# Kernel tuning notes

Hardware: AMD Instinct MI355X
Metric: run time of the kernel (lower is better)

The kernel has to match this reference:

```python
import jax, jax.numpy as jnp
import numpy as np

NUM_HEAD = 16
DIM_HEAD = 64
IN_DIM = NUM_HEAD * DIM_HEAD
SLEN = 1024
BSZ = 32
LN_EPS = 1e-5


def setup_inputs() -> dict:
    key = jax.random.key(0)
    ks = jax.random.split(key, 8)
    std = 1.0 / np.sqrt(DIM_HEAD)
    std_q = 0.01 / np.sqrt(DIM_HEAD)
    h = jax.random.normal(ks[0], (SLEN, BSZ, IN_DIM), dtype=jnp.float32)
    W_y = std * jax.random.normal(ks[1], (1, NUM_HEAD, DIM_HEAD, DIM_HEAD), dtype=jnp.float32)
    W_q = std_q * jax.random.normal(ks[2], (1, NUM_HEAD, DIM_HEAD, DIM_HEAD), dtype=jnp.float32)
    W_k = std * jax.random.normal(ks[3], (1, NUM_HEAD, DIM_HEAD, DIM_HEAD), dtype=jnp.float32)
    w_b = -1.0 + std * jax.random.normal(ks[4], (1, NUM_HEAD, DIM_HEAD, 4), dtype=jnp.float32)
    out_w = (1.0 / np.sqrt(IN_DIM)) * jax.random.normal(ks[5], (IN_DIM, IN_DIM), dtype=jnp.float32)  # (out, in), no bias
    ln_g = jnp.ones((IN_DIM,), dtype=jnp.float32)
    ln_b = jnp.zeros((IN_DIM,), dtype=jnp.float32)
    return {"h": h, "W_y": W_y, "W_q": W_q, "W_k": W_k, "w_b": w_b,
            "out_w": out_w, "ln_g": ln_g, "ln_b": ln_b}


def _layer_norm(x, g, b):
    mu = jnp.mean(x, axis=-1, keepdims=True)
    var = jnp.mean(jnp.square(x - mu), axis=-1, keepdims=True)
    return (x - mu) * jax.lax.rsqrt(var + LN_EPS) * g + b


def _srwm_forward(h, W_y, W_q, W_k, w_b, out_w, ln_g, ln_b):
    slen, bsz, in_dim = h.shape
    H, D = W_y.shape[1], W_y.shape[2]
    x = h.reshape(slen, bsz, H, D)  # (T,B,H,D) -- scan over leading T

    Wy0 = jnp.broadcast_to(W_y, (bsz, H, D, D))
    Wq0 = jnp.broadcast_to(W_q, (bsz, H, D, D))
    Wk0 = jnp.broadcast_to(W_k, (bsz, H, D, D))
    wb0 = jnp.broadcast_to(w_b, (bsz, H, D, 4))

    def step(carry, x_t):
        Wy, Wq, Wk, wb = carry  # (B,H,D,D) / (B,H,D,4)
        y = jnp.einsum('bhod,bhd->bho', Wy, x_t)
        q = jax.nn.softmax(jnp.einsum('bhod,bhd->bho', Wq, x_t), axis=-1)
        k = jax.nn.softmax(jnp.einsum('bhod,bhd->bho', Wk, x_t), axis=-1)
        beta = jax.nn.sigmoid(jnp.einsum('bhdk,bhd->bhk', wb, x_t))  # (B,H,4)
        # old values (keyed by k) and new target values (keyed by q)
        yk = jnp.einsum('bhod,bhd->bho', Wy, k); yq = jnp.einsum('bhod,bhd->bho', Wy, q)
        qk = jnp.einsum('bhod,bhd->bho', Wq, k); qq = jnp.einsum('bhod,bhd->bho', Wq, q)
        kk = jnp.einsum('bhod,bhd->bho', Wk, k); kq = jnp.einsum('bhod,bhd->bho', Wk, q)
        bk = jnp.einsum('bhdk,bhd->bhk', wb, k); bq = jnp.einsum('bhdk,bhd->bhk', wb, q)
        # delta-rule rank-1 self-modification, per-submatrix learned rate
        Wy = Wy + beta[..., 0, None, None] * ((yq - yk)[..., :, None] * k[..., None, :])
        Wq = Wq + beta[..., 1, None, None] * ((qq - qk)[..., :, None] * k[..., None, :])
        Wk = Wk + beta[..., 2, None, None] * ((kq - kk)[..., :, None] * k[..., None, :])
        wb = wb + beta[..., 3, None, None] * (k[..., :, None] * (bq - bk)[..., None, :])
        out_t = jax.nn.softmax(y, axis=-1)  # v0 applies softmax on y
        return (Wy, Wq, Wk, wb), out_t

    _, ys = jax.lax.scan(step, (Wy0, Wq0, Wk0, wb0), x)  # ys: (T,B,H,D)
    out = ys.reshape(slen, bsz, H * D)
    out = out @ out_w.T  # out_linear, no bias
    out = _layer_norm(h, ln_g, ln_b) + out  # use_ln + use_res
    return out


def reference(h, W_y, W_q, W_k, w_b, out_w, ln_g, ln_b):
    return _srwm_forward(h, W_y, W_q, W_k, w_b, out_w, ln_g, ln_b)
```

## Files before the change

kernel.cpp:

```cpp
#include <hip/hip_runtime.h>
#include <hip/hip_bf16.h>

#define SLEN 1024
#define BSZ 32
#define NHEAD 16
#define DHEAD 64
#define INDIM 1024

typedef __attribute__((ext_vector_type(8))) __bf16 bf16x8;
typedef __attribute__((ext_vector_type(4))) float f32x4;
typedef __attribute__((ext_vector_type(2))) float f32x2;

#if __has_builtin(__builtin_elementwise_fma)
__device__ __forceinline__ f32x2 pk_fma(f32x2 a, f32x2 b, f32x2 c) {
  return __builtin_elementwise_fma(a, b, c);
}
#else
__device__ __forceinline__ f32x2 pk_fma(f32x2 a, f32x2 b, f32x2 c) {
  f32x2 r; r.x = fmaf(a.x, b.x, c.x); r.y = fmaf(a.y, b.y, c.y); return r;
}
#endif

template <int C>
__device__ __forceinline__ float dppmov(float v) {
  return __int_as_float(__builtin_amdgcn_update_dpp(
      __float_as_int(v), __float_as_int(v), C, 0xF, 0xF, false));
}
__device__ __forceinline__ float wred_sum_u(float v) {
  v += dppmov<0x111>(v);
  v += dppmov<0x112>(v);
  v += dppmov<0x114>(v);
  v += dppmov<0x118>(v);
  v += dppmov<0x142>(v);
  v += dppmov<0x143>(v);
  return __int_as_float(__builtin_amdgcn_readlane(__float_as_int(v), 63));
}
__device__ __forceinline__ float wred_max_u(float v) {
  v = fmaxf(v, dppmov<0x111>(v));
  v = fmaxf(v, dppmov<0x112>(v));
  v = fmaxf(v, dppmov<0x114>(v));
  v = fmaxf(v, dppmov<0x118>(v));
  v = fmaxf(v, dppmov<0x142>(v));
  v = fmaxf(v, dppmov<0x143>(v));
  return __int_as_float(__builtin_amdgcn_readlane(__float_as_int(v), 63));
}

__global__ __launch_bounds__(256, 2) void srwm_scan(
    const float* __restrict__ h,
    const float* __restrict__ Wy0, const float* __restrict__ Wq0,
    const float* __restrict__ Wk0, const float* __restrict__ wb0,
    __hip_bfloat16* __restrict__ ys)
{
  const int p  = blockIdx.x;
  const int b  = p >> 4;
  const int hd = p & 15;
  const int tid = threadIdx.x;
  const int w = tid >> 6, l = tid & 63;

  __shared__ float sx[2][64];
  __shared__ float sq[2][64];
  __shared__ float sk[2][64];
  __shared__ float sbeta[2][4];

  f32x2 wrow[32];
  float xnext = 0.f;
  float cshift = 0.f;

  if (w < 3) {
    const float* base = (w == 0) ? Wy0 : (w == 1) ? Wq0 : Wk0;
    const float4* s4 = (const float4*)(base + (size_t)(hd * DHEAD + l) * DHEAD);
#pragma unroll
    for (int c = 0; c < 16; ++c) {
      const float4 v = s4[c];
      wrow[2 * c + 0] = f32x2{v.x, v.y};
      wrow[2 * c + 1] = f32x2{v.z, v.w};
    }
  } else {
    const float4 v = *(const float4*)(wb0 + (size_t)(hd * DHEAD + l) * 4);
    wrow[0] = f32x2{v.x, v.y};
    wrow[1] = f32x2{v.z, v.w};
    sx[0][l] = h[(size_t)b * INDIM + hd * DHEAD + l];
    xnext = h[(size_t)BSZ * INDIM + (size_t)b * INDIM + hd * DHEAD + l];
  }
  __syncthreads();

  const size_t xstride = (size_t)BSZ * INDIM;
  const float* xsrc = h + (size_t)b * INDIM + hd * DHEAD + l;
  __hip_bfloat16* ydst = ys + (size_t)b * INDIM + hd * DHEAD + l;

#pragma unroll 2
  for (int t = 0; t < SLEN; ++t) {
    const int cur = t & 1, nxt = cur ^ 1;
    if (w < 3) {
      const float* xb = sx[cur];
      f32x2 a0 = (f32x2)(0.f), a1 = (f32x2)(0.f);
#pragma unroll
      for (int c = 0; c < 16; ++c) {
        const float4 xc = *(const float4*)(xb + 4 * c);
        a0 = pk_fma(wrow[2 * c + 0], f32x2{xc.x, xc.y}, a0);
        a1 = pk_fma(wrow[2 * c + 1], f32x2{xc.z, xc.w}, a1);
      }
      const f32x2 as = a0 + a1;
      const float a = as.x + as.y;
      const float e = __expf(a - cshift);
      const float mnew = wred_max_u(a);
      const float s = wred_sum_u(e);
      const float sm = e * __builtin_amdgcn_rcpf(s);
      cshift = mnew;
      if (w == 0) {
        ydst[(size_t)t * xstride] = __float2bfloat16(sm);
      } else if (w == 1) {
        sq[cur][l] = sm;
      } else {
        sk[cur][l] = sm;
      }
    } else {
      sx[nxt][l] = xnext;
      const int tload = (t + 2 < SLEN) ? (t + 2) : (SLEN - 1);
      xnext = xsrc[(size_t)tload * xstride];
      const float xd = sx[cur][l];
      const float z0 = wred_sum_u(wrow[0].x * xd);
      const float z1 = wred_sum_u(wrow[0].y * xd);
      const float z2 = wred_sum_u(wrow[1].x * xd);
      const float z3 = wred_sum_u(wrow[1].y * xd);
      if (l == 0) {
        sbeta[cur][0] = __builtin_amdgcn_rcpf(1.f + __expf(-z0));
        sbeta[cur][1] = __builtin_amdgcn_rcpf(1.f + __expf(-z1));
        sbeta[cur][2] = __builtin_amdgcn_rcpf(1.f + __expf(-z2));
        sbeta[cur][3] = __builtin_amdgcn_rcpf(1.f + __expf(-z3));
      }
    }
    __syncthreads();
    if (w < 3) {
      const float* qb = sq[cur];
      const float* kb = sk[cur];
      const float beta = sbeta[cur][w];
      f32x2 kr[32];
      f32x2 d0 = (f32x2)(0.f), d1 = (f32x2)(0.f);
#pragma unroll
      for (int c = 0; c < 16; ++c) {
        const float4 q4 = *(const float4*)(qb + 4 * c);
        const float4 k4 = *(const float4*)(kb + 4 * c);
        const f32x2 klo = f32x2{k4.x, k4.y}, khi = f32x2{k4.z, k4.w};
        kr[2 * c + 0] = klo; kr[2 * c + 1] = khi;
        d0 = pk_fma(wrow[2 * c + 0], f32x2{q4.x, q4.y} - klo, d0);
        d1 = pk_fma(wrow[2 * c + 1], f32x2{q4.z, q4.w} - khi, d1);
      }
      const f32x2 dsum = d0 + d1;
      const float sc = beta * (dsum.x + dsum.y);
      const f32x2 scv = (f32x2)(sc);
#pragma unroll
      for (int c = 0; c < 32; ++c) wrow[c] = pk_fma(scv, kr[c], wrow[c]);
    } else {
      const float qd = sq[cur][l], kd = sk[cur][l];
      const float dd = qd - kd;
      const float z0 = wred_sum_u(wrow[0].x * dd);
      const float z1 = wred_sum_u(wrow[0].y * dd);
      const float z2 = wred_sum_u(wrow[1].x * dd);
      const float z3 = wred_sum_u(wrow[1].y * dd);
      const float s3 = sbeta[cur][3] * kd;
      wrow[0].x = fmaf(s3, z0, wrow[0].x);
      wrow[0].y = fmaf(s3, z1, wrow[0].y);
      wrow[1].x = fmaf(s3, z2, wrow[1].x);
      wrow[1].y = fmaf(s3, z3, wrow[1].y);
    }
  }
}

__global__ __launch_bounds__(256) void ln_stats(
    const float* __restrict__ h, float2* __restrict__ stats)
{
  const int row = blockIdx.x * 4 + (threadIdx.x >> 6);
  const int l = threadIdx.x & 63;
  const float4* hp = (const float4*)(h + (size_t)row * INDIM);
  float s = 0.f, s2 = 0.f;
#pragma unroll
  for (int c = 0; c < 4; ++c) {
    const float4 v = hp[c * 64 + l];
    s  += v.x + v.y + v.z + v.w;
    s2 += v.x * v.x + v.y * v.y + v.z * v.z + v.w * v.w;
  }
  s  = wred_sum_u(s);
  s2 = wred_sum_u(s2);
  if (l == 0) {
    const float mu  = s * (1.f / INDIM);
    const float var = s2 * (1.f / INDIM) - mu * mu;
    stats[row] = make_float2(mu, rsqrtf(var + 1e-5f));
  }
}

__global__ void cvt_bf16(const float* __restrict__ src,
                         __hip_bfloat16* __restrict__ dst, int n)
{
  const int i = blockIdx.x * blockDim.x + threadIdx.x;
  if (i < n) dst[i] = __float2bfloat16(src[i]);
}

__global__ __launch_bounds__(256) void gemm_ln(
    const __hip_bfloat16* __restrict__ A,
    const __hip_bfloat16* __restrict__ Bw,
    const float* __restrict__ h,
    const float2* __restrict__ stats,
    const float* __restrict__ g,
    const float* __restrict__ bvec,
    float* __restrict__ out)
{
  const int K = INDIM;
  __shared__ __align__(16) __hip_bfloat16 As[128 * 32];
  __shared__ __align__(16) __hip_bfloat16 Bs[128 * 32];
  const int tid = threadIdx.x, w = tid >> 6, l = tid & 63;
  const int wm = w >> 1, wn = w & 1;
  const int m0 = blockIdx.x * 128, n0 = blockIdx.y * 128;

  f32x4 acc[4][4];
#pragma unroll
  for (int i = 0; i < 4; ++i)
#pragma unroll
    for (int j = 0; j < 4; ++j) acc[i][j] = (f32x4)(0.f);

  const int mr = tid >> 2;
  const int kc = (tid & 3) * 8;

  for (int k0 = 0; k0 < K; k0 += 32) {
    const uint4 va0 = *(const uint4*)(A  + (size_t)(m0 + mr)      * K + k0 + kc);
    const uint4 va1 = *(const uint4*)(A  + (size_t)(m0 + mr + 64) * K + k0 + kc);
    const uint4 vb0 = *(const uint4*)(Bw + (size_t)(n0 + mr)      * K + k0 + kc);
    const uint4 vb1 = *(const uint4*)(Bw + (size_t)(n0 + mr + 64) * K + k0 + kc);
    *(uint4*)((char*)As + (size_t)tid * 16)         = va0;
    *(uint4*)((char*)As + (size_t)(tid + 256) * 16) = va1;
    *(uint4*)((char*)Bs + (size_t)tid * 16)         = vb0;
    *(uint4*)((char*)Bs + (size_t)(tid + 256) * 16) = vb1;
    __syncthreads();

    bf16x8 af[4], bfr[4];
    const int koff = (l >> 4) * 16;
#pragma unroll
    for (int i = 0; i < 4; ++i) {
      af[i]  = *(const bf16x8*)((const char*)As +
                 (size_t)(wm * 64 + i * 16 + (l & 15)) * 64 + koff);
      bfr[i] = *(const bf16x8*)((const char*)Bs +
                 (size_t)(wn * 64 + i * 16 + (l & 15)) * 64 + koff);
    }
#pragma unroll
    for (int i = 0; i < 4; ++i)
#pragma unroll
      for (int j = 0; j < 4; ++j)
        acc[i][j] = __builtin_amdgcn_mfma_f32_16x16x32_bf16(
            af[i], bfr[j], acc[i][j], 0, 0, 0);
    __syncthreads();
  }

  float gv[4], bv[4];
  int cols[4];
#pragma unroll
  for (int j = 0; j < 4; ++j) {
    const int col = n0 + wn * 64 + j * 16 + (l & 15);
    cols[j] = col; gv[j] = g[col]; bv[j] = bvec[col];
  }
#pragma unroll
  for (int i = 0; i < 4; ++i) {
#pragma unroll
    for (int r = 0; r < 4; ++r) {
      const int row = m0 + wm * 64 + i * 16 + (l >> 4) * 4 + r;
      const float2 st = stats[row];
      const float* hrow = h + (size_t)row * INDIM;
      float* orow = out + (size_t)row * INDIM;
#pragma unroll
      for (int j = 0; j < 4; ++j) {
        const float lnv = (hrow[cols[j]] - st.x) * st.y * gv[j] + bv[j];
        orow[cols[j]] = acc[i][j][r] + lnv;
      }
    }
  }
}

extern "C" void kernel_launch(void* const* d_in, const int* in_sizes, int n_in,
                              void* d_out, int out_size, void* d_ws, size_t ws_size,
                              hipStream_t stream)
{
  const float* h    = (const float*)d_in[0];
  const float* Wy   = (const float*)d_in[1];
  const float* Wq   = (const float*)d_in[2];
  const float* Wk   = (const float*)d_in[3];
  const float* wb   = (const float*)d_in[4];
  const float* outw = (const float*)d_in[5];
  const float* lng  = (const float*)d_in[6];
  const float* lnb  = (const float*)d_in[7];
  float* out = (float*)d_out;

  char* ws = (char*)d_ws;
  __hip_bfloat16* ys  = (__hip_bfloat16*)ws;
  __hip_bfloat16* wbf = (__hip_bfloat16*)(ws + 67108864);
  float2*       stats = (float2*)(ws + 67108864 + 2097152);

  cvt_bf16 <<<4096, 256, 0, stream>>>(outw, wbf, INDIM * INDIM);
  ln_stats <<<8192, 256, 0, stream>>>(h, stats);
  srwm_scan<<<512,  256, 0, stream>>>(h, Wy, Wq, Wk, wb, ys);
  gemm_ln  <<<dim3(256, 8), 256, 0, stream>>>(ys, wbf, h, stats, lng, lnb, out);
}
```

Baseline: 1.599 ms.

## Defer rank-1 weight update past barrier and batch bf16 output stores

The rank-1 weight update W += sc*k^T is postponed to the next step and applied after the matvec. The pending correction is added to the step's logits through a k·x dot product reduced across the wave, which takes the weight-update FMAs off the critical path between the two barriers. Softmax(y) outputs are staged in a shared buffer and written as 16-byte vectors every 8 steps, and the x prefetch load moves to the second phase. The dot-product loops also gain more independent accumulators. In exchange the kernel adds an extra wave reduction per step, keeps kr live across iterations (more VGPRs), and changes rounding order slightly.

```diff
diff --git a/kernel.cpp b/kernel.cpp
--- a/kernel.cpp
+++ b/kernel.cpp
@@ -61,8 +61,11 @@
   __shared__ float sq[2][64];
   __shared__ float sk[2][64];
   __shared__ float sbeta[2][4];
+  __shared__ __hip_bfloat16 ysbuf[8][64];
 
   f32x2 wrow[32];
+  f32x2 kr[32];
+  float sc_pend = 0.f;
   float xnext = 0.f;
   float cshift = 0.f;
 
@@ -75,6 +78,9 @@
       wrow[2 * c + 0] = f32x2{v.x, v.y};
       wrow[2 * c + 1] = f32x2{v.z, v.w};
     }
+#pragma unroll
+    for (int c = 0; c < 32; ++c) kr[c] = (f32x2)(0.f);
+    if (w == 2) sk[1][l] = 0.f;
   } else {
     const float4 v = *(const float4*)(wb0 + (size_t)(hd * DHEAD + l) * 4);
     wrow[0] = f32x2{v.x, v.y};
@@ -86,38 +92,45 @@
 
   const size_t xstride = (size_t)BSZ * INDIM;
   const float* xsrc = h + (size_t)b * INDIM + hd * DHEAD + l;
-  __hip_bfloat16* ydst = ys + (size_t)b * INDIM + hd * DHEAD + l;
+  __hip_bfloat16* ybase = ys + (size_t)b * INDIM + hd * DHEAD;
 
 #pragma unroll 2
   for (int t = 0; t < SLEN; ++t) {
-    const int cur = t & 1, nxt = cur ^ 1;
+    const int cur = t & 1, nxt = cur ^ 1, prev = nxt;
     if (w < 3) {
       const float* xb = sx[cur];
       f32x2 a0 = (f32x2)(0.f), a1 = (f32x2)(0.f);
-#pragma unroll
-      for (int c = 0; c < 16; ++c) {
-        const float4 xc = *(const float4*)(xb + 4 * c);
-        a0 = pk_fma(wrow[2 * c + 0], f32x2{xc.x, xc.y}, a0);
-        a1 = pk_fma(wrow[2 * c + 1], f32x2{xc.z, xc.w}, a1);
-      }
-      const f32x2 as = a0 + a1;
-      const float a = as.x + as.y;
+      f32x2 a2 = (f32x2)(0.f), a3 = (f32x2)(0.f);
+#pragma unroll
+      for (int c = 0; c < 8; ++c) {
+        const float4 x0 = *(const float4*)(xb + 8 * c);
+        const float4 x1 = *(const float4*)(xb + 8 * c + 4);
+        a0 = pk_fma(wrow[4 * c + 0], f32x2{x0.x, x0.y}, a0);
+        a1 = pk_fma(wrow[4 * c + 1], f32x2{x0.z, x0.w}, a1);
+        a2 = pk_fma(wrow[4 * c + 2], f32x2{x1.x, x1.y}, a2);
+        a3 = pk_fma(wrow[4 * c + 3], f32x2{x1.z, x1.w}, a3);
+      }
+      const f32x2 as = (a0 + a1) + (a2 + a3);
+      const float rl = sk[prev][l] * xb[l];
+      const float r  = wred_sum_u(rl);
+      const float a  = (as.x + as.y) + sc_pend * r;
       const float e = __expf(a - cshift);
       const float mnew = wred_max_u(a);
       const float s = wred_sum_u(e);
       const float sm = e * __builtin_amdgcn_rcpf(s);
       cshift = mnew;
       if (w == 0) {
-        ydst[(size_t)t * xstride] = __float2bfloat16(sm);
+        ysbuf[t & 7][l] = __float2bfloat16(sm);
       } else if (w == 1) {
         sq[cur][l] = sm;
       } else {
         sk[cur][l] = sm;
       }
+      const f32x2 spv = (f32x2)(sc_pend);
+#pragma unroll
+      for (int c = 0; c < 32; ++c) wrow[c] = pk_fma(spv, kr[c], wrow[c]);
     } else {
       sx[nxt][l] = xnext;
-      const int tload = (t + 2 < SLEN) ? (t + 2) : (SLEN - 1);
-      xnext = xsrc[(size_t)tload * xstride];
       const float xd = sx[cur][l];
       const float z0 = wred_sum_u(wrow[0].x * xd);
       const float z1 = wred_sum_u(wrow[0].y * xd);
@@ -132,26 +145,36 @@
     }
     __syncthreads();
     if (w < 3) {
+      if (w == 0 && (t & 7) == 7) {
+        const uint4 v = ((const uint4*)ysbuf)[l];
+        const int t0 = t - 7 + (l >> 3);
+        *(uint4*)(ybase + (size_t)t0 * xstride + (l & 7) * 8) = v;
+      }
       const float* qb = sq[cur];
       const float* kb = sk[cur];
       const float beta = sbeta[cur][w];
-      f32x2 kr[32];
       f32x2 d0 = (f32x2)(0.f), d1 = (f32x2)(0.f);
-#pragma unroll
-      for (int c = 0; c < 16; ++c) {
-        const float4 q4 = *(const float4*)(qb + 4 * c);
-        const float4 k4 = *(const float4*)(kb + 4 * c);
-        const f32x2 klo = f32x2{k4.x, k4.y}, khi = f32x2{k4.z, k4.w};
-        kr[2 * c + 0] = klo; kr[2 * c + 1] = khi;
-        d0 = pk_fma(wrow[2 * c + 0], f32x2{q4.x, q4.y} - klo, d0);
-        d1 = pk_fma(wrow[2 * c + 1], f32x2{q4.z, q4.w} - khi, d1);
-      }
-      const f32x2 dsum = d0 + d1;
-      const float sc = beta * (dsum.x + dsum.y);
-      const f32x2 scv = (f32x2)(sc);
-#pragma unroll
-      for (int c = 0; c < 32; ++c) wrow[c] = pk_fma(scv, kr[c], wrow[c]);
+      f32x2 d2 = (f32x2)(0.f), d3 = (f32x2)(0.f);
+#pragma unroll
+      for (int c = 0; c < 8; ++c) {
+        const float4 q0 = *(const float4*)(qb + 8 * c);
+        const float4 q1 = *(const float4*)(qb + 8 * c + 4);
+        const float4 k0 = *(const float4*)(kb + 8 * c);
+        const float4 k1 = *(const float4*)(kb + 8 * c + 4);
+        const f32x2 ka = f32x2{k0.x, k0.y}, kb2 = f32x2{k0.z, k0.w};
+        const f32x2 kc = f32x2{k1.x, k1.y}, kd = f32x2{k1.z, k1.w};
+        kr[4 * c + 0] = ka; kr[4 * c + 1] = kb2;
+        kr[4 * c + 2] = kc; kr[4 * c + 3] = kd;
+        d0 = pk_fma(wrow[4 * c + 0], f32x2{q0.x, q0.y} - ka,  d0);
+        d1 = pk_fma(wrow[4 * c + 1], f32x2{q0.z, q0.w} - kb2, d1);
+        d2 = pk_fma(wrow[4 * c + 2], f32x2{q1.x, q1.y} - kc,  d2);
+        d3 = pk_fma(wrow[4 * c + 3], f32x2{q1.z, q1.w} - kd,  d3);
+      }
+      const f32x2 ds = (d0 + d1) + (d2 + d3);
+      sc_pend = beta * (ds.x + ds.y);
     } else {
+      const int tload = (t + 2 < SLEN) ? (t + 2) : (SLEN - 1);
+      xnext = xsrc[(size_t)tload * xstride];
       const float qd = sq[cur][l], kd = sk[cur][l];
       const float dd = qd - kd;
       const float z0 = wred_sum_u(wrow[0].x * dd);
```

Result: no change. 1.625 ms (+1.7%).
